# Optimization experiments

Measured on AMD Instinct MI355X. Metric: run time of the kernel, lower is better.

Reference implementation:

```python
import jax, jax.numpy as jnp
import numpy as np

K_NEIGH = 16  # ball-query neighborhood size


def pdist2(a, b):
    # (B,N,3),(B,M,3) -> (B,N,M) squared euclidean distances
    aa = jnp.sum(a * a, -1)[:, :, None]
    bb = jnp.sum(b * b, -1)[:, None, :]
    return jnp.maximum(aa + bb - 2.0 * jnp.einsum('bnd,bmd->bnm', a, b), 0.0)


def fps(xyz, npoint):
    # furthest point sampling, xyz (B,N,3) -> idx (B,npoint) int32
    B, N, _ = xyz.shape

    def body(carry, _):
        dist, far = carry
        centroid = xyz[jnp.arange(B), far]  # (B,3)
        d = jnp.sum((xyz - centroid[:, None, :]) ** 2, -1)
        dist = jnp.minimum(dist, d)
        nxt = jnp.argmax(dist, axis=1).astype(jnp.int32)
        return (dist, nxt), far

    init = (jnp.full((B, N), 1e10, xyz.dtype), jnp.zeros((B,), jnp.int32))
    _, idxs = jax.lax.scan(body, init, None, length=npoint)
    return idxs.T  # (B, npoint)


def gather(x, idx):
    # x (B,N,C), idx (B,S) -> (B,S,C)
    return jnp.take_along_axis(x, idx[:, :, None], axis=1)


def lae_conv(xyz, fea, W, b, A, radius):
    # LAE-Conv: ball-query (K nearest capped to radius, out-of-ball -> self),
    # pointwise feature transform, attention over neighbors from coord offsets.
    B, N, _ = xyz.shape
    d2 = pdist2(xyz, xyz)
    negd, idx = jax.lax.top_k(-d2, K_NEIGH)          # (B,N,K)
    in_ball = (-negd) <= radius * radius
    self_idx = jnp.broadcast_to(jnp.arange(N, dtype=idx.dtype)[None, :, None], idx.shape)
    idx = jnp.where(in_ball, idx, self_idx)
    g_xyz = jnp.take_along_axis(xyz[:, None], idx[..., None], axis=2) - xyz[:, :, None, :]  # (B,N,K,3)
    g_fea = jnp.take_along_axis(fea[:, None], idx[..., None], axis=2)                        # (B,N,K,Cin)
    h = jnp.einsum('bnkc,co->bnko', g_fea, W) + b    # (B,N,K,Cout)
    alpha = jax.nn.softmax(jnp.einsum('bnkd,d->bnk', g_xyz, A), axis=-1)
    return jax.nn.relu(jnp.einsum('bnk,bnko->bno', alpha, h))


def self_attn(fea, Wq, Wk, Wv):
    # non-local self-attention block with additive merge (PSAB)
    q, k, v = fea @ Wq, fea @ Wk, fea @ Wv
    a = jax.nn.softmax(jnp.einsum('bnc,bmc->bnm', q, k), axis=-1)
    return jnp.einsum('bnm,bmc->bnc', a, v) + fea


def fp_interp(xyz_d, xyz_s, fea_d, fea_s):
    # pointnet feature propagation: 3-NN inverse-distance interp + skip concat
    d2 = pdist2(xyz_d, xyz_s)
    negd, idx = jax.lax.top_k(-d2, 3)
    w = 1.0 / jnp.maximum(-negd, 1e-10)
    w = w / jnp.sum(w, -1, keepdims=True)
    g = jnp.take_along_axis(fea_s[:, None], idx[..., None], axis=2)  # (B,Nd,3,C)
    interp = jnp.einsum('bnk,bnkc->bnc', w, g)
    return jnp.concatenate([fea_d, interp], axis=-1)


def pan_forward(xyz, W0, b0, A0, W1, b1, A1, W2, b2, A2, W3, b3, A3, W4, b4, A4,
                W5, b5, A5, W6, b6, A6, Wq1, Wk1, Wv1, Wq2, Wk2, Wv2, Wq3, Wk3, Wv3, Wf, bf):
    fea0 = lae_conv(xyz, xyz, W0, b0, A0, 0.06)       # (B,N,64)
    idx1 = fps(xyz, 512)
    xyz1, fea1 = gather(xyz, idx1), gather(fea0, idx1)
    fea1 = lae_conv(xyz1, fea1, W1, b1, A1, 0.12)     # (B,512,128)
    idx2 = fps(xyz1, 128)
    xyz2, fea2 = gather(xyz1, idx2), gather(fea1, idx2)
    fea2 = lae_conv(xyz2, fea2, W2, b2, A2, 0.3)      # (B,128,256)
    fea2 = self_attn(fea2, Wq1, Wk1, Wv1)
    idx3 = fps(xyz2, 64)
    xyz3, fea3 = gather(xyz2, idx3), gather(fea2, idx3)
    fea3 = lae_conv(xyz3, fea3, W3, b3, A3, 0.5)      # (B,64,512)
    fea3 = self_attn(fea3, Wq2, Wk2, Wv2)
    fea2 = fp_interp(xyz2, xyz3, fea2, fea3)          # (B,128,768)
    fea2 = lae_conv(xyz2, fea2, W4, b4, A4, 0.3)      # (B,128,256)
    fea2 = self_attn(fea2, Wq3, Wk3, Wv3)
    fea1 = fp_interp(xyz1, xyz2, fea1, fea2)          # (B,512,384)
    fea1 = lae_conv(xyz1, fea1, W5, b5, A5, 0.12)     # (B,512,256)
    fea0 = fp_interp(xyz, xyz1, fea0, fea1)           # (B,N,320)
    fea0 = lae_conv(xyz, fea0, W6, b6, A6, 0.06)      # (B,N,128)
    out = fea0 @ Wf + bf                              # (B,N,num_class)
    return out.transpose(0, 2, 1)                     # (B,num_class,N)


def setup_inputs() -> dict:
    key = jax.random.key(0)
    B, N, NUM_CLASS = 4, 4096, 13
    ks = iter(jax.random.split(key, 64))

    def lin(cin, cout):
        return jax.random.normal(next(ks), (cin, cout), jnp.float32) / np.sqrt(cin).astype(np.float32)

    inp = {'xyz': jax.random.uniform(next(ks), (B, N, 3), jnp.float32)}
    lae_dims = [(3, 64), (64, 128), (128, 256), (256, 512), (768, 256), (384, 256), (320, 128)]
    for i, (ci, co) in enumerate(lae_dims):
        inp[f'W{i}'] = lin(ci, co)
        inp[f'b{i}'] = jnp.zeros((co,), jnp.float32)
        inp[f'A{i}'] = jax.random.normal(next(ks), (3,), jnp.float32)
    for j, c in zip((1, 2, 3), (256, 512, 256)):
        inp[f'Wq{j}'] = lin(c, c)
        inp[f'Wk{j}'] = lin(c, c)
        inp[f'Wv{j}'] = lin(c, c)
    inp['Wf'] = lin(128, NUM_CLASS)
    inp['bf'] = jnp.zeros((NUM_CLASS,), jnp.float32)
    return inp


def reference(xyz, W0, b0, A0, W1, b1, A1, W2, b2, A2, W3, b3, A3, W4, b4, A4,
              W5, b5, A5, W6, b6, A6, Wq1, Wk1, Wv1, Wq2, Wk2, Wv2, Wq3, Wk3, Wv3, Wf, bf):
    return pan_forward(xyz, W0, b0, A0, W1, b1, A1, W2, b2, A2, W3, b3, A3, W4, b4, A4,
                       W5, b5, A5, W6, b6, A6, Wq1, Wk1, Wv1, Wq2, Wk2, Wv2, Wq3, Wk3, Wv3, Wf, bf)
```

## Files before the change

### kernel.cpp

```cpp
#include <hip/hip_runtime.h>
#include <math.h>

#define NB 4

typedef unsigned long long u64;

#define CSWAP(a, b)                                          \
  {                                                          \
    u64 _mn = (b < a) ? b : a;                               \
    u64 _mx = (b < a) ? a : b;                               \
    a = _mn;                                                 \
    b = _mx;                                                 \
  }

__global__ __launch_bounds__(256) void norms_kernel(const float* __restrict__ xyz,
                                                    float4* __restrict__ xw, int total) {
#pragma clang fp contract(off)
  int i = blockIdx.x * 256 + threadIdx.x;
  if (i >= total) return;
  float x = xyz[3 * i + 0], y = xyz[3 * i + 1], z = xyz[3 * i + 2];
  xw[i] = make_float4(x, y, z, x * x + y * y + z * z);
}

__device__ __forceinline__ void knn16_search(const float4* __restrict__ xwb, int N, int n,
                                             int lane, u64* lists, u64* win) {
#pragma clang fp contract(off)
  float4 q = xwb[n];
  float qq = q.w;
  const u64 SENT = ((u64)0x7F800000u << 32) | (unsigned)lane;
  u64 k0 = SENT, k1 = SENT, k2 = SENT, k3 = SENT, k4 = SENT, k5 = SENT, k6 = SENT,
      k7 = SENT, k8 = SENT, k9 = SENT, k10 = SENT, k11 = SENT, k12 = SENT, k13 = SENT,
      k14 = SENT, k15 = SENT;
  int rounds = N >> 6;
  for (int j = 0; j < rounds; ++j) {
    int m = j * 64 + lane;
    float4 p = xwb[m];
    float ab = q.x * p.x + q.y * p.y + q.z * p.z;
    float d2 = fmaxf((qq + p.w) - 2.0f * ab, 0.0f);
    u64 key = ((u64)__float_as_uint(d2) << 32) | (unsigned)m;
    if (key < k15) {
      k15 = key;
      CSWAP(k14, k15); CSWAP(k13, k14); CSWAP(k12, k13); CSWAP(k11, k12);
      CSWAP(k10, k11); CSWAP(k9, k10);  CSWAP(k8, k9);   CSWAP(k7, k8);
      CSWAP(k6, k7);   CSWAP(k5, k6);   CSWAP(k4, k5);   CSWAP(k3, k4);
      CSWAP(k2, k3);   CSWAP(k1, k2);   CSWAP(k0, k1);
    }
  }
  lists[0 * 64 + lane] = k0;   lists[1 * 64 + lane] = k1;
  lists[2 * 64 + lane] = k2;   lists[3 * 64 + lane] = k3;
  lists[4 * 64 + lane] = k4;   lists[5 * 64 + lane] = k5;
  lists[6 * 64 + lane] = k6;   lists[7 * 64 + lane] = k7;
  lists[8 * 64 + lane] = k8;   lists[9 * 64 + lane] = k9;
  lists[10 * 64 + lane] = k10; lists[11 * 64 + lane] = k11;
  lists[12 * 64 + lane] = k12; lists[13 * 64 + lane] = k13;
  lists[14 * 64 + lane] = k14; lists[15 * 64 + lane] = k15;
  __syncthreads();
  int head = 0;
  u64 outk = 0;
  for (int r = 0; r < 16; ++r) {
    u64 h = lists[head * 64 + lane];
    u64 mn = h;
#pragma unroll
    for (int mask = 32; mask; mask >>= 1) {
      u64 o = __shfl_xor(mn, mask);
      if (o < mn) mn = o;
    }
    if (h == mn) head++;
    if (lane == r) outk = mn;
  }
  if (lane < 16) win[lane] = outk;
  __syncthreads();
}

__device__ __forceinline__ void lae_alphas(const float4* __restrict__ xwb, int n,
                                           const int* idv, const float* __restrict__ A,
                                           float* al) {
  float ax = A[0], ay = A[1], az = A[2];
  float4 q = xwb[n];
  float mx = -3.0e38f;
#pragma unroll
  for (int k = 0; k < 16; ++k) {
    float4 p = xwb[idv[k]];
    float gx = p.x - q.x, gy = p.y - q.y, gz = p.z - q.z;
    float s = gx * ax + gy * ay + gz * az;
    al[k] = s;
    mx = fmaxf(mx, s);
  }
  float sum = 0.0f;
#pragma unroll
  for (int k = 0; k < 16; ++k) { al[k] = expf(al[k] - mx); sum += al[k]; }
#pragma unroll
  for (int k = 0; k < 16; ++k) al[k] = al[k] / sum;
}

template <int NT, int PTS, int NPT>
__device__ __forceinline__ void fps_body(const float4* __restrict__ xw, int N, int npoint,
                                         int* __restrict__ idx_out,
                                         float4* __restrict__ xw_out, u64* smem, int b,
                                         int tid) {
#pragma clang fp contract(off)
  constexpr int NW = NT / 64;
  u64* rk = smem;
  int* hist = (int*)(smem + 2 * NW);
  float* sxyz = (float*)(hist + 512);
  const float4* xb = xw + (size_t)b * N;
  for (int i = tid; i < N; i += NT) {
    float4 p = xb[i];
    sxyz[3 * i + 0] = p.x;
    sxyz[3 * i + 1] = p.y;
    sxyz[3 * i + 2] = p.z;
  }
  float px[PTS], py[PTS], pz[PTS], dist[PTS];
#pragma unroll
  for (int p = 0; p < PTS; ++p) {
    float4 v = xb[tid + p * NT];
    px[p] = v.x;
    py[p] = v.y;
    pz[p] = v.z;
    dist[p] = 1e10f;
  }
  __syncthreads();
  int far = 0;
  float cx = sxyz[0], cy = sxyz[1], cz = sxyz[2];
  for (int t = 0; t < npoint; ++t) {
    if (tid == 0) hist[t] = far;
    u64 K[PTS];
#pragma unroll
    for (int p = 0; p < PTS; ++p) {
      float dx = px[p] - cx, dy = py[p] - cy, dz = pz[p] - cz;
      float d = dx * dx + dy * dy + dz * dz;
      float nd = fminf(dist[p], d);
      dist[p] = nd;
      K[p] = ((u64)__float_as_uint(nd) << 32) | (unsigned)(~(tid + p * NT));
    }
#pragma unroll
    for (int s = PTS / 2; s >= 1; s >>= 1) {
#pragma unroll
      for (int i = 0; i < s; ++i)
        if (K[i + s] > K[i]) K[i] = K[i + s];
    }
    u64 key = K[0];
#pragma unroll
    for (int m = 1; m <= 32; m <<= 1) {
      u64 o = __shfl_xor(key, m);
      if (o > key) key = o;
    }
    if constexpr (NW > 1) {
      int par = (t & 1) * NW;
      if ((tid & 63) == 0) rk[par + (tid >> 6)] = key;
      __syncthreads();
      key = rk[par + 0];
#pragma unroll
      for (int w = 1; w < NW; ++w)
        if (rk[par + w] > key) key = rk[par + w];
    }
    far = (int)(~(unsigned)key);
    cx = sxyz[3 * far + 0];
    cy = sxyz[3 * far + 1];
    cz = sxyz[3 * far + 2];
  }
  __syncthreads();
  for (int s = tid; s < npoint; s += NT) {
    int idp = hist[s];
    idx_out[(size_t)b * npoint + s] = idp;
    xw_out[(size_t)b * npoint + s] = xb[idp];
  }
}

__device__ __forceinline__ void knn_gw_body(const float4* __restrict__ xw_s, int N, float r2,
                                            int* __restrict__ idxK,
                                            const int* __restrict__ srcmap,
                                            const float* __restrict__ fea_src, int Nsrc,
                                            int Cin, const float* __restrict__ A,
                                            float* __restrict__ wf, int bn, int lane,
                                            u64* lists, u64* win) {
  int b = bn / N, n = bn - b * N;
  const float4* xb = xw_s + (size_t)b * N;
  knn16_search(xb, N, n, lane, lists, win);
  int idv[16];
#pragma unroll
  for (int k = 0; k < 16; ++k) {
    u64 kk = win[k];
    float d2 = __uint_as_float((unsigned)(kk >> 32));
    idv[k] = (d2 <= r2) ? (int)(kk & 0xFFFFFFFFu) : n;
  }
  if (lane < 16) idxK[(size_t)bn * 16 + lane] = idv[lane];
  float al[16];
  lae_alphas(xb, n, idv, A, al);
  int row[16];
  const int* sm = srcmap + (size_t)b * N;
#pragma unroll
  for (int k = 0; k < 16; ++k) row[k] = sm[idv[k]];
  const float* fb = fea_src + (size_t)b * Nsrc * Cin;
  float* wo = wf + (size_t)bn * Cin;
  for (int c = lane; c < Cin; c += 64) {
    float acc = 0.0f;
#pragma unroll
    for (int k = 0; k < 16; ++k) acc += al[k] * fb[(size_t)row[k] * Cin + c];
    wo[c] = acc;
  }
}

__device__ __forceinline__ void knn_gw0_body(const float4* __restrict__ xw, int N, float r2,
                                             int* __restrict__ idxK,
                                             const float* __restrict__ W0,
                                             const float* __restrict__ b0,
                                             const float* __restrict__ A0,
                                             float* __restrict__ fea0, int bn, int lane,
                                             u64* lists, u64* win) {
  int b = bn / N, n = bn - b * N;
  const float4* xb = xw + (size_t)b * N;
  knn16_search(xb, N, n, lane, lists, win);
  int idv[16];
#pragma unroll
  for (int k = 0; k < 16; ++k) {
    u64 kk = win[k];
    float d2 = __uint_as_float((unsigned)(kk >> 32));
    idv[k] = (d2 <= r2) ? (int)(kk & 0xFFFFFFFFu) : n;
  }
  if (lane < 16) idxK[(size_t)bn * 16 + lane] = idv[lane];
  float al[16];
  lae_alphas(xb, n, idv, A0, al);
  float w0 = 0.0f, w1 = 0.0f, w2 = 0.0f;
#pragma unroll
  for (int k = 0; k < 16; ++k) {
    float4 p = xb[idv[k]];
    w0 += al[k] * p.x;
    w1 += al[k] * p.y;
    w2 += al[k] * p.z;
  }
  float v = w0 * W0[0 * 64 + lane] + w1 * W0[1 * 64 + lane] + w2 * W0[2 * 64 + lane] +
            b0[lane];
  fea0[(size_t)bn * 64 + lane] = fmaxf(v, 0.0f);
}

__device__ __forceinline__ void interp3_body(const float4* __restrict__ xd,
                                             const float4* __restrict__ xs, int Nd, int Ns,
                                             int* __restrict__ idx3, float* __restrict__ w3,
                                             int gid) {
#pragma clang fp contract(off)
  int b = gid / Nd;
  const float4* xb = xs + (size_t)b * Ns;
  float4 q = xd[gid];
  float qq = q.w;
  float v0 = 3.0e38f, v1 = 3.0e38f, v2 = 3.0e38f;
  int i0 = 0, i1 = 0, i2 = 0;
  for (int m = 0; m < Ns; ++m) {
    float4 p = xb[m];
    float ab = q.x * p.x + q.y * p.y + q.z * p.z;
    float d2 = fmaxf((qq + p.w) - 2.0f * ab, 0.0f);
    if (d2 < v2) {
      if (d2 < v0) { v2 = v1; i2 = i1; v1 = v0; i1 = i0; v0 = d2; i0 = m; }
      else if (d2 < v1) { v2 = v1; i2 = i1; v1 = d2; i1 = m; }
      else { v2 = d2; i2 = m; }
    }
  }
  float w0 = 1.0f / fmaxf(v0, 1e-10f);
  float w1 = 1.0f / fmaxf(v1, 1e-10f);
  float w2 = 1.0f / fmaxf(v2, 1e-10f);
  float s = w0 + w1 + w2;
  idx3[gid * 3 + 0] = i0; idx3[gid * 3 + 1] = i1; idx3[gid * 3 + 2] = i2;
  w3[gid * 3 + 0] = w0 / s; w3[gid * 3 + 1] = w1 / s; w3[gid * 3 + 2] = w2 / s;
}

__global__ __launch_bounds__(256) void combo_A_kernel(
    const float4* __restrict__ xw0, float r2, int* __restrict__ idxK0,
    const float* __restrict__ W0, const float* __restrict__ b0,
    const float* __restrict__ A0, float* __restrict__ fea0, int* __restrict__ idx1,
    float4* __restrict__ xw1) {
  __shared__ u64 smem[6432];
  if (blockIdx.x < NB) {
    fps_body<256, 16, 4096>(xw0, 4096, 512, idx1, xw1, smem, blockIdx.x, threadIdx.x);
  } else {
    int wave = threadIdx.x >> 6, lane = threadIdx.x & 63;
    int bn = (blockIdx.x - NB) * 4 + wave;
    knn_gw0_body(xw0, 4096, r2, idxK0, W0, b0, A0, fea0, bn, lane, smem + (size_t)wave * 1024,
                 smem + 4096 + wave * 16);
  }
}

__global__ __launch_bounds__(64) void combo_B_kernel(
    const float4* __restrict__ xw0, const float4* __restrict__ xw1, float r2,
    int* __restrict__ idxK1, const int* __restrict__ idx1, const float* __restrict__ fea0,
    const float* __restrict__ A1, float* __restrict__ wf, int* __restrict__ idx2,
    float4* __restrict__ xw2, int* __restrict__ idxI0, float* __restrict__ wI0) {
  __shared__ u64 smem[1056];
  int bid = blockIdx.x;
  if (bid < NB) {
    fps_body<64, 8, 512>(xw1, 512, 128, idx2, xw2, smem, bid, threadIdx.x);
  } else if (bid < NB + NB * 512) {
    knn_gw_body(xw1, 512, r2, idxK1, idx1, fea0, 4096, 64, A1, wf, bid - NB, threadIdx.x,
                smem, smem + 1024);
  } else {
    int gid = (bid - NB - NB * 512) * 64 + threadIdx.x;
    interp3_body(xw0, xw1, 4096, 512, idxI0, wI0, gid);
  }
}

__global__ __launch_bounds__(64) void combo_D_kernel(
    const float4* __restrict__ xw1, const float4* __restrict__ xw2, float r2,
    int* __restrict__ idxK2, const int* __restrict__ idx2, const float* __restrict__ fea1,
    const float* __restrict__ A2, float* __restrict__ wf, int* __restrict__ idx3,
    float4* __restrict__ xw3, int* __restrict__ idxI1, float* __restrict__ wI1) {
  __shared__ u64 smem[1056];
  int bid = blockIdx.x;
  if (bid < NB) {
    fps_body<64, 2, 128>(xw2, 128, 64, idx3, xw3, smem, bid, threadIdx.x);
  } else if (bid < NB + NB * 128) {
    knn_gw_body(xw2, 128, r2, idxK2, idx2, fea1, 512, 128, A2, wf, bid - NB, threadIdx.x,
                smem, smem + 1024);
  } else {
    int gid = (bid - NB - NB * 128) * 64 + threadIdx.x;
    interp3_body(xw1, xw2, 512, 128, idxI1, wI1, gid);
  }
}

__global__ __launch_bounds__(64) void combo_H_kernel(
    const float4* __restrict__ xw2, const float4* __restrict__ xw3, float r2,
    int* __restrict__ idxK3, const int* __restrict__ idx3, const float* __restrict__ fea2b,
    const float* __restrict__ A3, float* __restrict__ wf, int* __restrict__ idxI2,
    float* __restrict__ wI2) {
  __shared__ u64 smem[1056];
  int bid = blockIdx.x;
  if (bid < NB * 64) {
    knn_gw_body(xw3, 64, r2, idxK3, idx3, fea2b, 128, 256, A3, wf, bid, threadIdx.x, smem,
                smem + 1024);
  } else {
    int gid = (bid - NB * 64) * 64 + threadIdx.x;
    interp3_body(xw2, xw3, 128, 64, idxI2, wI2, gid);
  }
}

__global__ __launch_bounds__(64) void gwpost_kernel(const float4* __restrict__ xw,
                                                    const float* __restrict__ Y,
                                                    const int* __restrict__ knn,
                                                    const float* __restrict__ A,
                                                    const float* __restrict__ bias,
                                                    float* __restrict__ out, int N, int C) {
  int bn = blockIdx.x;
  int b = bn / N, n = bn - b * N;
  int lane = threadIdx.x;
  const float4* xb = xw + (size_t)b * N;
  const int* kn = knn + (size_t)bn * 16;
  int idv[16];
#pragma unroll
  for (int k = 0; k < 16; ++k) idv[k] = kn[k];
  float al[16];
  lae_alphas(xb, n, idv, A, al);
  const float* Yb = Y + (size_t)b * N * C;
  float* wo = out + (size_t)bn * C;
  for (int c = lane; c < C; c += 64) {
    float acc = 0.0f;
#pragma unroll
    for (int k = 0; k < 16; ++k) acc += al[k] * Yb[(size_t)idv[k] * C + c];
    wo[c] = fmaxf(acc + bias[c], 0.0f);
  }
}

__global__ __launch_bounds__(64) void gwpost_final_kernel(
    const float4* __restrict__ xw, const float* __restrict__ Y, const int* __restrict__ knn,
    const float* __restrict__ A, const float* __restrict__ bias,
    const float* __restrict__ Wf, const float* __restrict__ bfv, float* __restrict__ out,
    int N) {
  int bn = blockIdx.x;
  int b = bn / N, n = bn - b * N;
  int lane = threadIdx.x;
  const float4* xb = xw + (size_t)b * N;
  const int* kn = knn + (size_t)bn * 16;
  int idv[16];
#pragma unroll
  for (int k = 0; k < 16; ++k) idv[k] = kn[k];
  float al[16];
  lae_alphas(xb, n, idv, A, al);
  const float* Yb = Y + (size_t)b * N * 128;
  float a0 = 0.0f, a1 = 0.0f;
#pragma unroll
  for (int k = 0; k < 16; ++k) {
    const float* yr = Yb + (size_t)idv[k] * 128;
    a0 += al[k] * yr[lane];
    a1 += al[k] * yr[lane + 64];
  }
  float v0 = fmaxf(a0 + bias[lane], 0.0f);
  float v1 = fmaxf(a1 + bias[lane + 64], 0.0f);
  float* ob = out + ((size_t)b * 13) * N + n;
#pragma unroll
  for (int cls = 0; cls < 13; ++cls) {
    float p = v0 * Wf[lane * 13 + cls] + v1 * Wf[(lane + 64) * 13 + cls];
#pragma unroll
    for (int m = 32; m; m >>= 1) p += __shfl_xor(p, m);
    if (lane == 0) ob[(size_t)cls * N] = p + bfv[cls];
  }
}

__device__ __forceinline__ void gemm_body(const float* __restrict__ Amat,
                                          const float* __restrict__ W,
                                          const float* __restrict__ bias,
                                          float* __restrict__ out, int K, int Cout, int relu,
                                          const int* __restrict__ i3,
                                          const float* __restrict__ w3,
                                          const float* __restrict__ Zb, int Nd, int Ns,
                                          float* lds_a) {
  int co = blockIdx.x * 64 + (threadIdx.x & 63);
  int rg = threadIdx.x >> 6;
  int r0 = blockIdx.y * 32;
  float acc[8];
#pragma unroll
  for (int j = 0; j < 8; ++j) acc[j] = 0.0f;
  for (int k0 = 0; k0 < K; k0 += 32) {
    int row = threadIdx.x >> 3;
    int kq = (threadIdx.x & 7) * 4;
    int gk = k0 + kq;
    const float* ap = Amat + (size_t)(r0 + row) * K + gk;
    float a0 = 0.0f, a1 = 0.0f, a2 = 0.0f, a3 = 0.0f;
    if (gk + 3 < K) {
      float4 tv = *(const float4*)ap;
      a0 = tv.x; a1 = tv.y; a2 = tv.z; a3 = tv.w;
    } else {
      if (gk + 0 < K) a0 = ap[0];
      if (gk + 1 < K) a1 = ap[1];
      if (gk + 2 < K) a2 = ap[2];
    }
    __syncthreads();
    lds_a[(kq + 0) * 36 + row] = a0;
    lds_a[(kq + 1) * 36 + row] = a1;
    lds_a[(kq + 2) * 36 + row] = a2;
    lds_a[(kq + 3) * 36 + row] = a3;
    __syncthreads();
    int kmax = K - k0;
    if (kmax > 32) kmax = 32;
    if (kmax == 32) {
#pragma unroll
      for (int kk = 0; kk < 32; ++kk) {
        float w = W[(size_t)(k0 + kk) * Cout + co];
        const float* ar = &lds_a[kk * 36 + rg * 8];
        float4 x0 = *(const float4*)ar;
        float4 x1 = *(const float4*)(ar + 4);
        acc[0] += x0.x * w; acc[1] += x0.y * w; acc[2] += x0.z * w; acc[3] += x0.w * w;
        acc[4] += x1.x * w; acc[5] += x1.y * w; acc[6] += x1.z * w; acc[7] += x1.w * w;
      }
    } else {
      for (int kk = 0; kk < kmax; ++kk) {
        float w = W[(size_t)(k0 + kk) * Cout + co];
        const float* ar = &lds_a[kk * 36 + rg * 8];
        float4 x0 = *(const float4*)ar;
        float4 x1 = *(const float4*)(ar + 4);
        acc[0] += x0.x * w; acc[1] += x0.y * w; acc[2] += x0.z * w; acc[3] += x0.w * w;
        acc[4] += x1.x * w; acc[5] += x1.y * w; acc[6] += x1.z * w; acc[7] += x1.w * w;
      }
    }
  }
  float bb = bias ? bias[co] : 0.0f;
#pragma unroll
  for (int j = 0; j < 8; ++j) {
    int r = r0 + rg * 8 + j;
    float vv = acc[j] + bb;
    if (i3) {
      int bidx = r / Nd;
      const int* ii = i3 + (size_t)r * 3;
      const float* ww = w3 + (size_t)r * 3;
      const float* zb = Zb + (size_t)bidx * Ns * Cout;
      vv += ww[0] * zb[(size_t)ii[0] * Cout + co] + ww[1] * zb[(size_t)ii[1] * Cout + co] +
            ww[2] * zb[(size_t)ii[2] * Cout + co];
    }
    if (relu) vv = fmaxf(vv, 0.0f);
    out[(size_t)r * Cout + co] = vv;
  }
}

__global__ __launch_bounds__(256) void gemm_kernel(const float* __restrict__ Amat,
                                                   const float* __restrict__ W,
                                                   const float* __restrict__ bias,
                                                   float* __restrict__ out, int K, int Cout,
                                                   int relu, const int* __restrict__ i3,
                                                   const float* __restrict__ w3,
                                                   const float* __restrict__ Zb, int Nd,
                                                   int Ns) {
  __shared__ float lds_a[32 * 36];
  gemm_body(Amat, W, bias, out, K, Cout, relu, i3, w3, Zb, Nd, Ns, lds_a);
}

__global__ __launch_bounds__(256) void gemm_qkv_kernel(
    const float* __restrict__ Amat, const float* __restrict__ Wq,
    const float* __restrict__ Wk, const float* __restrict__ Wv, float* __restrict__ oq,
    float* __restrict__ ok, float* __restrict__ ov, int K, int Cout) {
  __shared__ float lds_a[32 * 36];
  const float* W = blockIdx.z == 0 ? Wq : (blockIdx.z == 1 ? Wk : Wv);
  float* o = blockIdx.z == 0 ? oq : (blockIdx.z == 1 ? ok : ov);
  gemm_body(Amat, W, nullptr, o, K, Cout, 0, nullptr, nullptr, nullptr, 0, 0, lds_a);
}

__global__ __launch_bounds__(128) void attn_kernel(const float* __restrict__ q,
                                                   const float* __restrict__ k,
                                                   const float* __restrict__ v,
                                                   const float* __restrict__ fea,
                                                   float* __restrict__ out, int N, int C) {
  __shared__ float sa[128];
  __shared__ float sb[128];
  int b = blockIdx.y, n = blockIdx.x, t = threadIdx.x;
  const float* qn = q + ((size_t)b * N + n) * C;
  if (t < N) {
    const float4* km = (const float4*)(k + ((size_t)b * N + t) * C);
    const float4* q4 = (const float4*)qn;
    float acc = 0.0f;
    int C4 = C >> 2;
    for (int c = 0; c < C4; ++c) {
      float4 kv = km[c];
      float4 qv = q4[c];
      acc += qv.x * kv.x + qv.y * kv.y + qv.z * kv.z + qv.w * kv.w;
    }
    sa[t] = acc;
  }
  __syncthreads();
  float mx = -3.0e38f;
  for (int i = 0; i < N; ++i) mx = fmaxf(mx, sa[i]);
  if (t < N) sb[t] = expf(sa[t] - mx);
  __syncthreads();
  float sum = 0.0f;
  for (int i = 0; i < N; ++i) sum += sb[i];
  size_t rowo = ((size_t)b * N + n) * C;
  for (int c = t; c < C; c += 128) {
    float acc = 0.0f;
    for (int m = 0; m < N; ++m) acc += sb[m] * v[((size_t)b * N + m) * C + c];
    out[rowo + c] = acc / sum + fea[rowo + c];
  }
}

extern "C" void kernel_launch(void* const* d_in, const int* in_sizes, int n_in,
                              void* d_out, int out_size, void* d_ws, size_t ws_size,
                              hipStream_t stream) {
  (void)in_sizes; (void)n_in; (void)out_size; (void)ws_size;
  const float* xyz = (const float*)d_in[0];
  const float* W[7]; const float* bi[7]; const float* A[7];
  for (int i = 0; i < 7; ++i) {
    W[i] = (const float*)d_in[1 + 3 * i];
    bi[i] = (const float*)d_in[2 + 3 * i];
    A[i] = (const float*)d_in[3 + 3 * i];
  }
  const float* Wq1 = (const float*)d_in[22];
  const float* Wk1 = (const float*)d_in[23];
  const float* Wv1 = (const float*)d_in[24];
  const float* Wq2 = (const float*)d_in[25];
  const float* Wk2 = (const float*)d_in[26];
  const float* Wv2 = (const float*)d_in[27];
  const float* Wq3 = (const float*)d_in[28];
  const float* Wk3 = (const float*)d_in[29];
  const float* Wv3 = (const float*)d_in[30];
  const float* Wf = (const float*)d_in[31];
  const float* bf = (const float*)d_in[32];
  float* out = (float*)d_out;

  const int B = NB, N0 = 4096, N1 = 512, N2 = 128, N3 = 64;
  char* base = (char*)d_ws;
  size_t off = 0;
  auto alloc = [&](size_t bytes) -> void* {
    void* p = base + off;
    off += (bytes + 255) & ~(size_t)255;
    return p;
  };
  float4* xw0 = (float4*)alloc((size_t)B * N0 * 16);
  float4* xw1 = (float4*)alloc((size_t)B * N1 * 16);
  float4* xw2 = (float4*)alloc((size_t)B * N2 * 16);
  float4* xw3 = (float4*)alloc((size_t)B * N3 * 16);
  int* idxK0 = (int*)alloc((size_t)B * N0 * 16 * 4);
  int* idxK1 = (int*)alloc((size_t)B * N1 * 16 * 4);
  int* idxK2 = (int*)alloc((size_t)B * N2 * 16 * 4);
  int* idxK3 = (int*)alloc((size_t)B * N3 * 16 * 4);
  int* idx1 = (int*)alloc((size_t)B * N1 * 4);
  int* idx2 = (int*)alloc((size_t)B * N2 * 4);
  int* idx3 = (int*)alloc((size_t)B * N3 * 4);
  float* fea0 = (float*)alloc((size_t)B * N0 * 64 * 4);
  float* fea1 = (float*)alloc((size_t)B * N1 * 128 * 4);
  float* fea1b = (float*)alloc((size_t)B * N1 * 256 * 4);
  float* fea2a = (float*)alloc((size_t)B * N2 * 256 * 4);
  float* fea2b = (float*)alloc((size_t)B * N2 * 256 * 4);
  float* fea2c = (float*)alloc((size_t)B * N2 * 256 * 4);
  float* fea2d = (float*)alloc((size_t)B * N2 * 256 * 4);
  float* fea3a = (float*)alloc((size_t)B * N3 * 512 * 4);
  float* fea3b = (float*)alloc((size_t)B * N3 * 512 * 4);
  float* qb = (float*)alloc((size_t)B * 32768 * 4);
  float* kb = (float*)alloc((size_t)B * 32768 * 4);
  float* vb = (float*)alloc((size_t)B * 32768 * 4);
  int* idxI2 = (int*)alloc((size_t)B * N2 * 3 * 4);
  float* wI2 = (float*)alloc((size_t)B * N2 * 3 * 4);
  int* idxI1 = (int*)alloc((size_t)B * N1 * 3 * 4);
  float* wI1 = (float*)alloc((size_t)B * N1 * 3 * 4);
  int* idxI0 = (int*)alloc((size_t)B * N0 * 3 * 4);
  float* wI0 = (float*)alloc((size_t)B * N0 * 3 * 4);
  float* Zb4 = (float*)alloc((size_t)B * N3 * 256 * 4);
  float* Zb5 = (float*)alloc((size_t)B * N2 * 256 * 4);
  float* Zb6 = (float*)alloc((size_t)B * N1 * 128 * 4);
  float* Y4 = (float*)alloc((size_t)B * N2 * 256 * 4);
  float* Y5 = (float*)alloc((size_t)B * N1 * 256 * 4);
  float* Y6 = (float*)alloc((size_t)B * N0 * 128 * 4);
  float* wfb = (float*)alloc((size_t)B * N0 * 320 * 4);

  float r2_0 = (float)(0.06 * 0.06);
  float r2_1 = (float)(0.12 * 0.12);
  float r2_2 = (float)(0.3 * 0.3);
  float r2_3 = (float)(0.5 * 0.5);

  norms_kernel<<<B * N0 / 256, 256, 0, stream>>>(xyz, xw0, B * N0);

  combo_A_kernel<<<B + B * N0 / 4, 256, 0, stream>>>(xw0, r2_0, idxK0, W[0], bi[0], A[0],
                                                     fea0, idx1, xw1);
  combo_B_kernel<<<B + B * N1 + B * N0 / 64, 64, 0, stream>>>(
      xw0, xw1, r2_1, idxK1, idx1, fea0, A[1], wfb, idx2, xw2, idxI0, wI0);
  gemm_kernel<<<dim3(2, B * N1 / 32), 256, 0, stream>>>(wfb, W[1], bi[1], fea1, 64, 128, 1,
                                                        nullptr, nullptr, nullptr, 0, 0);
  combo_D_kernel<<<B + B * N2 + B * N1 / 64, 64, 0, stream>>>(
      xw1, xw2, r2_2, idxK2, idx2, fea1, A[2], wfb, idx3, xw3, idxI1, wI1);
  gemm_kernel<<<dim3(4, B * N2 / 32), 256, 0, stream>>>(wfb, W[2], bi[2], fea2a, 128, 256, 1,
                                                        nullptr, nullptr, nullptr, 0, 0);
  gemm_qkv_kernel<<<dim3(4, B * N2 / 32, 3), 256, 0, stream>>>(fea2a, Wq1, Wk1, Wv1, qb, kb,
                                                               vb, 256, 256);
  attn_kernel<<<dim3(N2, B), 128, 0, stream>>>(qb, kb, vb, fea2a, fea2b, N2, 256);

  combo_H_kernel<<<B * N3 + B * N2 / 64, 64, 0, stream>>>(xw2, xw3, r2_3, idxK3, idx3, fea2b,
                                                          A[3], wfb, idxI2, wI2);
  gemm_kernel<<<dim3(8, B * N3 / 32), 256, 0, stream>>>(wfb, W[3], bi[3], fea3a, 256, 512, 1,
                                                        nullptr, nullptr, nullptr, 0, 0);
  gemm_qkv_kernel<<<dim3(8, B * N3 / 32, 3), 256, 0, stream>>>(fea3a, Wq2, Wk2, Wv2, qb, kb,
                                                               vb, 512, 512);
  attn_kernel<<<dim3(N3, B), 128, 0, stream>>>(qb, kb, vb, fea3a, fea3b, N3, 512);

  gemm_kernel<<<dim3(4, B * N3 / 32), 256, 0, stream>>>(fea3b, W[4] + 256 * 256, nullptr, Zb4,
                                                        512, 256, 0, nullptr, nullptr,
                                                        nullptr, 0, 0);
  gemm_kernel<<<dim3(4, B * N2 / 32), 256, 0, stream>>>(fea2b, W[4], nullptr, Y4, 256, 256, 0,
                                                        idxI2, wI2, Zb4, N2, N3);
  gwpost_kernel<<<B * N2, 64, 0, stream>>>(xw2, Y4, idxK2, A[4], bi[4], fea2c, N2, 256);
  gemm_qkv_kernel<<<dim3(4, B * N2 / 32, 3), 256, 0, stream>>>(fea2c, Wq3, Wk3, Wv3, qb, kb,
                                                               vb, 256, 256);
  attn_kernel<<<dim3(N2, B), 128, 0, stream>>>(qb, kb, vb, fea2c, fea2d, N2, 256);

  gemm_kernel<<<dim3(4, B * N2 / 32), 256, 0, stream>>>(fea2d, W[5] + 128 * 256, nullptr, Zb5,
                                                        256, 256, 0, nullptr, nullptr,
                                                        nullptr, 0, 0);
  gemm_kernel<<<dim3(4, B * N1 / 32), 256, 0, stream>>>(fea1, W[5], nullptr, Y5, 128, 256, 0,
                                                        idxI1, wI1, Zb5, N1, N2);
  gwpost_kernel<<<B * N1, 64, 0, stream>>>(xw1, Y5, idxK1, A[5], bi[5], fea1b, N1, 256);

  gemm_kernel<<<dim3(2, B * N1 / 32), 256, 0, stream>>>(fea1b, W[6] + 64 * 128, nullptr, Zb6,
                                                        256, 128, 0, nullptr, nullptr,
                                                        nullptr, 0, 0);
  gemm_kernel<<<dim3(2, B * N0 / 32), 256, 0, stream>>>(fea0, W[6], nullptr, Y6, 64, 128, 0,
                                                        idxI0, wI0, Zb6, N0, N1);
  gwpost_final_kernel<<<B * N0, 64, 0, stream>>>(xw0, Y6, idxK0, A[6], bi[6], Wf, bf, out,
                                                 N0);
}
```

Baseline: 916.2 us.

## Hoist skip-branch GEMMs into earlier combo kernels and rework FPS argmax

The skip-connection GEMMs (fea0·W6a, fea1·W5a, fea2b·W4a) move out of the decoder and run as extra blocks inside the earlier combo kernels, where they overlap with FPS and kNN work. The interpolation add becomes a separate elementwise kernel applied after the coarse GEMM. Combo B, D and H switch to 256-thread blocks with four waves each. FPS now gives each thread a contiguous run of points and finds the argmax with a float max-shuffle plus a ballot, instead of reducing packed 64-bit keys. The cost is three extra launches and an extra read-modify-write pass over Y.

Result: faster. 861.1 us, median of 2 (-6.0%).

```diff
diff --git a/kernel.cpp b/kernel.cpp
--- a/kernel.cpp
+++ b/kernel.cpp
@@ -100,6 +100,7 @@
                                          int tid) {
 #pragma clang fp contract(off)
   constexpr int NW = NT / 64;
+  constexpr bool FULL = (NT * PTS == NPT);
   u64* rk = smem;
   int* hist = (int*)(smem + 2 * NW);
   float* sxyz = (float*)(hist + 512);
@@ -113,10 +114,13 @@
   float px[PTS], py[PTS], pz[PTS], dist[PTS];
 #pragma unroll
   for (int p = 0; p < PTS; ++p) {
-    float4 v = xb[tid + p * NT];
-    px[p] = v.x;
-    py[p] = v.y;
-    pz[p] = v.z;
+    int pt = tid * PTS + p;
+    if (FULL || pt < N) {
+      float4 v = xb[pt];
+      px[p] = v.x;
+      py[p] = v.y;
+      pz[p] = v.z;
+    }
     dist[p] = 1e10f;
   }
   __syncthreads();
@@ -124,35 +128,38 @@
   float cx = sxyz[0], cy = sxyz[1], cz = sxyz[2];
   for (int t = 0; t < npoint; ++t) {
     if (tid == 0) hist[t] = far;
-    u64 K[PTS];
+    float bestd = -1.0f;
+    int bestp = 0;
 #pragma unroll
     for (int p = 0; p < PTS; ++p) {
-      float dx = px[p] - cx, dy = py[p] - cy, dz = pz[p] - cz;
-      float d = dx * dx + dy * dy + dz * dz;
-      float nd = fminf(dist[p], d);
-      dist[p] = nd;
-      K[p] = ((u64)__float_as_uint(nd) << 32) | (unsigned)(~(tid + p * NT));
-    }
-#pragma unroll
-    for (int s = PTS / 2; s >= 1; s >>= 1) {
-#pragma unroll
-      for (int i = 0; i < s; ++i)
-        if (K[i + s] > K[i]) K[i] = K[i + s];
-    }
-    u64 key = K[0];
-#pragma unroll
-    for (int m = 1; m <= 32; m <<= 1) {
-      u64 o = __shfl_xor(key, m);
-      if (o > key) key = o;
-    }
+      int pt = tid * PTS + p;
+      if (FULL || pt < N) {
+        float dx = px[p] - cx, dy = py[p] - cy, dz = pz[p] - cz;
+        float d = dx * dx + dy * dy + dz * dz;
+        float nd = fminf(dist[p], d);
+        dist[p] = nd;
+        if (nd > bestd) { bestd = nd; bestp = pt; }
+      }
+    }
+    float wmax = bestd;
+#pragma unroll
+    for (int m = 1; m <= 32; m <<= 1) wmax = fmaxf(wmax, __shfl_xor(wmax, m));
+    u64 mask = __ballot(bestd == wmax);
+    int wl = __ffsll(mask) - 1;
+    int widx = __shfl(bestp, wl);
+    u64 key = (wmax < 0.0f)
+                  ? 0ull
+                  : (((u64)__float_as_uint(wmax) << 32) | (unsigned)(~widx));
     if constexpr (NW > 1) {
       int par = (t & 1) * NW;
       if ((tid & 63) == 0) rk[par + (tid >> 6)] = key;
       __syncthreads();
       key = rk[par + 0];
 #pragma unroll
-      for (int w = 1; w < NW; ++w)
-        if (rk[par + w] > key) key = rk[par + w];
+      for (int w = 1; w < NW; ++w) {
+        u64 o = rk[par + w];
+        if (o > key) key = o;
+      }
     }
     far = (int)(~(unsigned)key);
     cx = sxyz[3 * far + 0];
@@ -263,146 +270,14 @@
   w3[gid * 3 + 0] = w0 / s; w3[gid * 3 + 1] = w1 / s; w3[gid * 3 + 2] = w2 / s;
 }
 
-__global__ __launch_bounds__(256) void combo_A_kernel(
-    const float4* __restrict__ xw0, float r2, int* __restrict__ idxK0,
-    const float* __restrict__ W0, const float* __restrict__ b0,
-    const float* __restrict__ A0, float* __restrict__ fea0, int* __restrict__ idx1,
-    float4* __restrict__ xw1) {
-  __shared__ u64 smem[6432];
-  if (blockIdx.x < NB) {
-    fps_body<256, 16, 4096>(xw0, 4096, 512, idx1, xw1, smem, blockIdx.x, threadIdx.x);
-  } else {
-    int wave = threadIdx.x >> 6, lane = threadIdx.x & 63;
-    int bn = (blockIdx.x - NB) * 4 + wave;
-    knn_gw0_body(xw0, 4096, r2, idxK0, W0, b0, A0, fea0, bn, lane, smem + (size_t)wave * 1024,
-                 smem + 4096 + wave * 16);
-  }
-}
-
-__global__ __launch_bounds__(64) void combo_B_kernel(
-    const float4* __restrict__ xw0, const float4* __restrict__ xw1, float r2,
-    int* __restrict__ idxK1, const int* __restrict__ idx1, const float* __restrict__ fea0,
-    const float* __restrict__ A1, float* __restrict__ wf, int* __restrict__ idx2,
-    float4* __restrict__ xw2, int* __restrict__ idxI0, float* __restrict__ wI0) {
-  __shared__ u64 smem[1056];
-  int bid = blockIdx.x;
-  if (bid < NB) {
-    fps_body<64, 8, 512>(xw1, 512, 128, idx2, xw2, smem, bid, threadIdx.x);
-  } else if (bid < NB + NB * 512) {
-    knn_gw_body(xw1, 512, r2, idxK1, idx1, fea0, 4096, 64, A1, wf, bid - NB, threadIdx.x,
-                smem, smem + 1024);
-  } else {
-    int gid = (bid - NB - NB * 512) * 64 + threadIdx.x;
-    interp3_body(xw0, xw1, 4096, 512, idxI0, wI0, gid);
-  }
-}
-
-__global__ __launch_bounds__(64) void combo_D_kernel(
-    const float4* __restrict__ xw1, const float4* __restrict__ xw2, float r2,
-    int* __restrict__ idxK2, const int* __restrict__ idx2, const float* __restrict__ fea1,
-    const float* __restrict__ A2, float* __restrict__ wf, int* __restrict__ idx3,
-    float4* __restrict__ xw3, int* __restrict__ idxI1, float* __restrict__ wI1) {
-  __shared__ u64 smem[1056];
-  int bid = blockIdx.x;
-  if (bid < NB) {
-    fps_body<64, 2, 128>(xw2, 128, 64, idx3, xw3, smem, bid, threadIdx.x);
-  } else if (bid < NB + NB * 128) {
-    knn_gw_body(xw2, 128, r2, idxK2, idx2, fea1, 512, 128, A2, wf, bid - NB, threadIdx.x,
-                smem, smem + 1024);
-  } else {
-    int gid = (bid - NB - NB * 128) * 64 + threadIdx.x;
-    interp3_body(xw1, xw2, 512, 128, idxI1, wI1, gid);
-  }
-}
-
-__global__ __launch_bounds__(64) void combo_H_kernel(
-    const float4* __restrict__ xw2, const float4* __restrict__ xw3, float r2,
-    int* __restrict__ idxK3, const int* __restrict__ idx3, const float* __restrict__ fea2b,
-    const float* __restrict__ A3, float* __restrict__ wf, int* __restrict__ idxI2,
-    float* __restrict__ wI2) {
-  __shared__ u64 smem[1056];
-  int bid = blockIdx.x;
-  if (bid < NB * 64) {
-    knn_gw_body(xw3, 64, r2, idxK3, idx3, fea2b, 128, 256, A3, wf, bid, threadIdx.x, smem,
-                smem + 1024);
-  } else {
-    int gid = (bid - NB * 64) * 64 + threadIdx.x;
-    interp3_body(xw2, xw3, 128, 64, idxI2, wI2, gid);
-  }
-}
-
-__global__ __launch_bounds__(64) void gwpost_kernel(const float4* __restrict__ xw,
-                                                    const float* __restrict__ Y,
-                                                    const int* __restrict__ knn,
-                                                    const float* __restrict__ A,
-                                                    const float* __restrict__ bias,
-                                                    float* __restrict__ out, int N, int C) {
-  int bn = blockIdx.x;
-  int b = bn / N, n = bn - b * N;
-  int lane = threadIdx.x;
-  const float4* xb = xw + (size_t)b * N;
-  const int* kn = knn + (size_t)bn * 16;
-  int idv[16];
-#pragma unroll
-  for (int k = 0; k < 16; ++k) idv[k] = kn[k];
-  float al[16];
-  lae_alphas(xb, n, idv, A, al);
-  const float* Yb = Y + (size_t)b * N * C;
-  float* wo = out + (size_t)bn * C;
-  for (int c = lane; c < C; c += 64) {
-    float acc = 0.0f;
-#pragma unroll
-    for (int k = 0; k < 16; ++k) acc += al[k] * Yb[(size_t)idv[k] * C + c];
-    wo[c] = fmaxf(acc + bias[c], 0.0f);
-  }
-}
-
-__global__ __launch_bounds__(64) void gwpost_final_kernel(
-    const float4* __restrict__ xw, const float* __restrict__ Y, const int* __restrict__ knn,
-    const float* __restrict__ A, const float* __restrict__ bias,
-    const float* __restrict__ Wf, const float* __restrict__ bfv, float* __restrict__ out,
-    int N) {
-  int bn = blockIdx.x;
-  int b = bn / N, n = bn - b * N;
-  int lane = threadIdx.x;
-  const float4* xb = xw + (size_t)b * N;
-  const int* kn = knn + (size_t)bn * 16;
-  int idv[16];
-#pragma unroll
-  for (int k = 0; k < 16; ++k) idv[k] = kn[k];
-  float al[16];
-  lae_alphas(xb, n, idv, A, al);
-  const float* Yb = Y + (size_t)b * N * 128;
-  float a0 = 0.0f, a1 = 0.0f;
-#pragma unroll
-  for (int k = 0; k < 16; ++k) {
-    const float* yr = Yb + (size_t)idv[k] * 128;
-    a0 += al[k] * yr[lane];
-    a1 += al[k] * yr[lane + 64];
-  }
-  float v0 = fmaxf(a0 + bias[lane], 0.0f);
-  float v1 = fmaxf(a1 + bias[lane + 64], 0.0f);
-  float* ob = out + ((size_t)b * 13) * N + n;
-#pragma unroll
-  for (int cls = 0; cls < 13; ++cls) {
-    float p = v0 * Wf[lane * 13 + cls] + v1 * Wf[(lane + 64) * 13 + cls];
-#pragma unroll
-    for (int m = 32; m; m >>= 1) p += __shfl_xor(p, m);
-    if (lane == 0) ob[(size_t)cls * N] = p + bfv[cls];
-  }
-}
-
-__device__ __forceinline__ void gemm_body(const float* __restrict__ Amat,
+__device__ __forceinline__ void gemm_body(int bx, int by, const float* __restrict__ Amat,
                                           const float* __restrict__ W,
                                           const float* __restrict__ bias,
                                           float* __restrict__ out, int K, int Cout, int relu,
-                                          const int* __restrict__ i3,
-                                          const float* __restrict__ w3,
-                                          const float* __restrict__ Zb, int Nd, int Ns,
                                           float* lds_a) {
-  int co = blockIdx.x * 64 + (threadIdx.x & 63);
+  int co = bx * 64 + (threadIdx.x & 63);
   int rg = threadIdx.x >> 6;
-  int r0 = blockIdx.y * 32;
+  int r0 = by * 32;
   float acc[8];
 #pragma unroll
   for (int j = 0; j < 8; ++j) acc[j] = 0.0f;
@@ -454,14 +329,6 @@
   for (int j = 0; j < 8; ++j) {
     int r = r0 + rg * 8 + j;
     float vv = acc[j] + bb;
-    if (i3) {
-      int bidx = r / Nd;
-      const int* ii = i3 + (size_t)r * 3;
-      const float* ww = w3 + (size_t)r * 3;
-      const float* zb = Zb + (size_t)bidx * Ns * Cout;
-      vv += ww[0] * zb[(size_t)ii[0] * Cout + co] + ww[1] * zb[(size_t)ii[1] * Cout + co] +
-            ww[2] * zb[(size_t)ii[2] * Cout + co];
-    }
     if (relu) vv = fmaxf(vv, 0.0f);
     out[(size_t)r * Cout + co] = vv;
   }
@@ -471,12 +338,9 @@
                                                    const float* __restrict__ W,
                                                    const float* __restrict__ bias,
                                                    float* __restrict__ out, int K, int Cout,
-                                                   int relu, const int* __restrict__ i3,
-                                                   const float* __restrict__ w3,
-                                                   const float* __restrict__ Zb, int Nd,
-                                                   int Ns) {
+                                                   int relu) {
   __shared__ float lds_a[32 * 36];
-  gemm_body(Amat, W, bias, out, K, Cout, relu, i3, w3, Zb, Nd, Ns, lds_a);
+  gemm_body(blockIdx.x, blockIdx.y, Amat, W, bias, out, K, Cout, relu, lds_a);
 }
 
 __global__ __launch_bounds__(256) void gemm_qkv_kernel(
@@ -486,7 +350,170 @@
   __shared__ float lds_a[32 * 36];
   const float* W = blockIdx.z == 0 ? Wq : (blockIdx.z == 1 ? Wk : Wv);
   float* o = blockIdx.z == 0 ? oq : (blockIdx.z == 1 ? ok : ov);
-  gemm_body(Amat, W, nullptr, o, K, Cout, 0, nullptr, nullptr, nullptr, 0, 0, lds_a);
+  gemm_body(blockIdx.x, blockIdx.y, Amat, W, nullptr, o, K, Cout, 0, lds_a);
+}
+
+__global__ __launch_bounds__(256) void interp_add_kernel(float* __restrict__ Y,
+                                                         const int* __restrict__ i3,
+                                                         const float* __restrict__ w3,
+                                                         const float* __restrict__ Zb,
+                                                         int Nd, int Ns, int C, int total) {
+  int gid = blockIdx.x * 256 + threadIdx.x;
+  if (gid >= total) return;
+  int c = gid % C;
+  int r = gid / C;
+  int b = r / Nd;
+  const int* ii = i3 + (size_t)r * 3;
+  const float* ww = w3 + (size_t)r * 3;
+  const float* zb = Zb + (size_t)b * Ns * C;
+  Y[gid] += ww[0] * zb[(size_t)ii[0] * C + c] + ww[1] * zb[(size_t)ii[1] * C + c] +
+            ww[2] * zb[(size_t)ii[2] * C + c];
+}
+
+__global__ __launch_bounds__(256) void combo_A_kernel(
+    const float4* __restrict__ xw0, float r2, int* __restrict__ idxK0,
+    const float* __restrict__ W0, const float* __restrict__ b0,
+    const float* __restrict__ A0, float* __restrict__ fea0, int* __restrict__ idx1,
+    float4* __restrict__ xw1) {
+  __shared__ u64 smem[6432];
+  if (blockIdx.x < NB) {
+    fps_body<256, 16, 4096>(xw0, 4096, 512, idx1, xw1, smem, blockIdx.x, threadIdx.x);
+  } else {
+    int wave = threadIdx.x >> 6, lane = threadIdx.x & 63;
+    int bn = (blockIdx.x - NB) * 4 + wave;
+    knn_gw0_body(xw0, 4096, r2, idxK0, W0, b0, A0, fea0, bn, lane, smem + (size_t)wave * 1024,
+                 smem + 4096 + wave * 16);
+  }
+}
+
+__global__ __launch_bounds__(256) void combo_B_kernel(
+    const float4* __restrict__ xw0, const float4* __restrict__ xw1, float r2,
+    int* __restrict__ idxK1, const int* __restrict__ idx1, const float* __restrict__ fea0,
+    const float* __restrict__ A1, float* __restrict__ wf, int* __restrict__ idx2,
+    float4* __restrict__ xw2, int* __restrict__ idxI0, float* __restrict__ wI0,
+    const float* __restrict__ W6a, float* __restrict__ Y6) {
+  __shared__ u64 smem[4160];
+  int bid = blockIdx.x;
+  if (bid < NB) {
+    fps_body<256, 2, 512>(xw1, 512, 128, idx2, xw2, smem, bid, threadIdx.x);
+  } else if (bid < NB + 512) {
+    int wave = threadIdx.x >> 6, lane = threadIdx.x & 63;
+    int bn = (bid - NB) * 4 + wave;
+    knn_gw_body(xw1, 512, r2, idxK1, idx1, fea0, 4096, 64, A1, wf, bn, lane,
+                smem + (size_t)wave * 1024, smem + 4096 + wave * 16);
+  } else if (bid < NB + 512 + 64) {
+    int gid = (bid - NB - 512) * 256 + threadIdx.x;
+    interp3_body(xw0, xw1, 4096, 512, idxI0, wI0, gid);
+  } else {
+    int gb = bid - (NB + 512 + 64);
+    gemm_body(gb & 1, gb >> 1, fea0, W6a, nullptr, Y6, 64, 128, 0, (float*)smem);
+  }
+}
+
+__global__ __launch_bounds__(256) void combo_D_kernel(
+    const float4* __restrict__ xw1, const float4* __restrict__ xw2, float r2,
+    int* __restrict__ idxK2, const int* __restrict__ idx2, const float* __restrict__ fea1,
+    const float* __restrict__ A2, float* __restrict__ wf, int* __restrict__ idx3,
+    float4* __restrict__ xw3, int* __restrict__ idxI1, float* __restrict__ wI1,
+    const float* __restrict__ W5a, float* __restrict__ Y5) {
+  __shared__ u64 smem[4160];
+  int bid = blockIdx.x;
+  if (bid < NB) {
+    fps_body<256, 1, 128>(xw2, 128, 64, idx3, xw3, smem, bid, threadIdx.x);
+  } else if (bid < NB + 128) {
+    int wave = threadIdx.x >> 6, lane = threadIdx.x & 63;
+    int bn = (bid - NB) * 4 + wave;
+    knn_gw_body(xw2, 128, r2, idxK2, idx2, fea1, 512, 128, A2, wf, bn, lane,
+                smem + (size_t)wave * 1024, smem + 4096 + wave * 16);
+  } else if (bid < NB + 128 + 8) {
+    int gid = (bid - NB - 128) * 256 + threadIdx.x;
+    interp3_body(xw1, xw2, 512, 128, idxI1, wI1, gid);
+  } else {
+    int gb = bid - (NB + 128 + 8);
+    gemm_body(gb & 3, gb >> 2, fea1, W5a, nullptr, Y5, 128, 256, 0, (float*)smem);
+  }
+}
+
+__global__ __launch_bounds__(256) void combo_H_kernel(
+    const float4* __restrict__ xw2, const float4* __restrict__ xw3, float r2,
+    int* __restrict__ idxK3, const int* __restrict__ idx3, const float* __restrict__ fea2b,
+    const float* __restrict__ A3, float* __restrict__ wf, int* __restrict__ idxI2,
+    float* __restrict__ wI2, const float* __restrict__ W4a, float* __restrict__ Y4) {
+  __shared__ u64 smem[4160];
+  int bid = blockIdx.x;
+  if (bid < 64) {
+    int wave = threadIdx.x >> 6, lane = threadIdx.x & 63;
+    int bn = bid * 4 + wave;
+    knn_gw_body(xw3, 64, r2, idxK3, idx3, fea2b, 128, 256, A3, wf, bn, lane,
+                smem + (size_t)wave * 1024, smem + 4096 + wave * 16);
+  } else if (bid < 64 + 2) {
+    int gid = (bid - 64) * 256 + threadIdx.x;
+    interp3_body(xw2, xw3, 128, 64, idxI2, wI2, gid);
+  } else {
+    int gb = bid - 66;
+    gemm_body(gb & 3, gb >> 2, fea2b, W4a, nullptr, Y4, 256, 256, 0, (float*)smem);
+  }
+}
+
+__global__ __launch_bounds__(64) void gwpost_kernel(const float4* __restrict__ xw,
+                                                    const float* __restrict__ Y,
+                                                    const int* __restrict__ knn,
+                                                    const float* __restrict__ A,
+                                                    const float* __restrict__ bias,
+                                                    float* __restrict__ out, int N, int C) {
+  int bn = blockIdx.x;
+  int b = bn / N, n = bn - b * N;
+  int lane = threadIdx.x;
+  const float4* xb = xw + (size_t)b * N;
+  const int* kn = knn + (size_t)bn * 16;
+  int idv[16];
+#pragma unroll
+  for (int k = 0; k < 16; ++k) idv[k] = kn[k];
+  float al[16];
+  lae_alphas(xb, n, idv, A, al);
+  const float* Yb = Y + (size_t)b * N * C;
+  float* wo = out + (size_t)bn * C;
+  for (int c = lane; c < C; c += 64) {
+    float acc = 0.0f;
+#pragma unroll
+    for (int k = 0; k < 16; ++k) acc += al[k] * Yb[(size_t)idv[k] * C + c];
+    wo[c] = fmaxf(acc + bias[c], 0.0f);
+  }
+}
+
+__global__ __launch_bounds__(64) void gwpost_final_kernel(
+    const float4* __restrict__ xw, const float* __restrict__ Y, const int* __restrict__ knn,
+    const float* __restrict__ A, const float* __restrict__ bias,
+    const float* __restrict__ Wf, const float* __restrict__ bfv, float* __restrict__ out,
+    int N) {
+  int bn = blockIdx.x;
+  int b = bn / N, n = bn - b * N;
+  int lane = threadIdx.x;
+  const float4* xb = xw + (size_t)b * N;
+  const int* kn = knn + (size_t)bn * 16;
+  int idv[16];
+#pragma unroll
+  for (int k = 0; k < 16; ++k) idv[k] = kn[k];
+  float al[16];
+  lae_alphas(xb, n, idv, A, al);
+  const float* Yb = Y + (size_t)b * N * 128;
+  float a0 = 0.0f, a1 = 0.0f;
+#pragma unroll
+  for (int k = 0; k < 16; ++k) {
+    const float* yr = Yb + (size_t)idv[k] * 128;
+    a0 += al[k] * yr[lane];
+    a1 += al[k] * yr[lane + 64];
+  }
+  float v0 = fmaxf(a0 + bias[lane], 0.0f);
+  float v1 = fmaxf(a1 + bias[lane + 64], 0.0f);
+  float* ob = out + ((size_t)b * 13) * N + n;
+#pragma unroll
+  for (int cls = 0; cls < 13; ++cls) {
+    float p = v0 * Wf[lane * 13 + cls] + v1 * Wf[(lane + 64) * 13 + cls];
+#pragma unroll
+    for (int m = 32; m; m >>= 1) p += __shfl_xor(p, m);
+    if (lane == 0) ob[(size_t)cls * N] = p + bfv[cls];
+  }
 }
 
 __global__ __launch_bounds__(128) void attn_kernel(const float* __restrict__ q,
@@ -603,48 +630,42 @@
 
   combo_A_kernel<<<B + B * N0 / 4, 256, 0, stream>>>(xw0, r2_0, idxK0, W[0], bi[0], A[0],
                                                      fea0, idx1, xw1);
-  combo_B_kernel<<<B + B * N1 + B * N0 / 64, 64, 0, stream>>>(
-      xw0, xw1, r2_1, idxK1, idx1, fea0, A[1], wfb, idx2, xw2, idxI0, wI0);
-  gemm_kernel<<<dim3(2, B * N1 / 32), 256, 0, stream>>>(wfb, W[1], bi[1], fea1, 64, 128, 1,
-                                                        nullptr, nullptr, nullptr, 0, 0);
-  combo_D_kernel<<<B + B * N2 + B * N1 / 64, 64, 0, stream>>>(
-      xw1, xw2, r2_2, idxK2, idx2, fea1, A[2], wfb, idx3, xw3, idxI1, wI1);
-  gemm_kernel<<<dim3(4, B * N2 / 32), 256, 0, stream>>>(wfb, W[2], bi[2], fea2a, 128, 256, 1,
-                                                        nullptr, nullptr, nullptr, 0, 0);
+  combo_B_kernel<<<NB + 512 + 64 + 1024, 256, 0, stream>>>(
+      xw0, xw1, r2_1, idxK1, idx1, fea0, A[1], wfb, idx2, xw2, idxI0, wI0, W[6], Y6);
+  gemm_kernel<<<dim3(2, B * N1 / 32), 256, 0, stream>>>(wfb, W[1], bi[1], fea1, 64, 128, 1);
+  combo_D_kernel<<<NB + 128 + 8 + 256, 256, 0, stream>>>(
+      xw1, xw2, r2_2, idxK2, idx2, fea1, A[2], wfb, idx3, xw3, idxI1, wI1, W[5], Y5);
+  gemm_kernel<<<dim3(4, B * N2 / 32), 256, 0, stream>>>(wfb, W[2], bi[2], fea2a, 128, 256, 1);
   gemm_qkv_kernel<<<dim3(4, B * N2 / 32, 3), 256, 0, stream>>>(fea2a, Wq1, Wk1, Wv1, qb, kb,
                                                                vb, 256, 256);
   attn_kernel<<<dim3(N2, B), 128, 0, stream>>>(qb, kb, vb, fea2a, fea2b, N2, 256);
 
-  combo_H_kernel<<<B * N3 + B * N2 / 64, 64, 0, stream>>>(xw2, xw3, r2_3, idxK3, idx3, fea2b,
-                                                          A[3], wfb, idxI2, wI2);
-  gemm_kernel<<<dim3(8, B * N3 / 32), 256, 0, stream>>>(wfb, W[3], bi[3], fea3a, 256, 512, 1,
-                                                        nullptr, nullptr, nullptr, 0, 0);
+  combo_H_kernel<<<64 + 2 + 64, 256, 0, stream>>>(xw2, xw3, r2_3, idxK3, idx3, fea2b, A[3],
+                                                  wfb, idxI2, wI2, W[4], Y4);
+  gemm_kernel<<<dim3(8, B * N3 / 32), 256, 0, stream>>>(wfb, W[3], bi[3], fea3a, 256, 512, 1);
   gemm_qkv_kernel<<<dim3(8, B * N3 / 32, 3), 256, 0, stream>>>(fea3a, Wq2, Wk2, Wv2, qb, kb,
                                                                vb, 512, 512);
   attn_kernel<<<dim3(N3, B), 128, 0, stream>>>(qb, kb, vb, fea3a, fea3b, N3, 512);
 
   gemm_kernel<<<dim3(4, B * N3 / 32), 256, 0, stream>>>(fea3b, W[4] + 256 * 256, nullptr, Zb4,
-                                                        512, 256, 0, nullptr, nullptr,
-                                                        nullptr, 0, 0);
-  gemm_kernel<<<dim3(4, B * N2 / 32), 256, 0, stream>>>(fea2b, W[4], nullptr, Y4, 256, 256, 0,
-                                                        idxI2, wI2, Zb4, N2, N3);
+                                                        512, 256, 0);
+  interp_add_kernel<<<B * N2 * 256 / 256, 256, 0, stream>>>(Y4, idxI2, wI2, Zb4, N2, N3, 256,
+                                                            B * N2 * 256);
   gwpost_kernel<<<B * N2, 64, 0, stream>>>(xw2, Y4, idxK2, A[4], bi[4], fea2c, N2, 256);
   gemm_qkv_kernel<<<dim3(4, B * N2 / 32, 3), 256, 0, stream>>>(fea2c, Wq3, Wk3, Wv3, qb, kb,
                                                                vb, 256, 256);
   attn_kernel<<<dim3(N2, B), 128, 0, stream>>>(qb, kb, vb, fea2c, fea2d, N2, 256);
 
   gemm_kernel<<<dim3(4, B * N2 / 32), 256, 0, stream>>>(fea2d, W[5] + 128 * 256, nullptr, Zb5,
-                                                        256, 256, 0, nullptr, nullptr,
-                                                        nullptr, 0, 0);
-  gemm_kernel<<<dim3(4, B * N1 / 32), 256, 0, stream>>>(fea1, W[5], nullptr, Y5, 128, 256, 0,
-                                                        idxI1, wI1, Zb5, N1, N2);
+                                                        256, 256, 0);
+  interp_add_kernel<<<B * N1 * 256 / 256, 256, 0, stream>>>(Y5, idxI1, wI1, Zb5, N1, N2, 256,
+                                                            B * N1 * 256);
   gwpost_kernel<<<B * N1, 64, 0, stream>>>(xw1, Y5, idxK1, A[5], bi[5], fea1b, N1, 256);
 
   gemm_kernel<<<dim3(2, B * N1 / 32), 256, 0, stream>>>(fea1b, W[6] + 64 * 128, nullptr, Zb6,
-                                                        256, 128, 0, nullptr, nullptr,
-                                                        nullptr, 0, 0);
-  gemm_kernel<<<dim3(2, B * N0 / 32), 256, 0, stream>>>(fea0, W[6], nullptr, Y6, 64, 128, 0,
-                                                        idxI0, wI0, Zb6, N0, N1);
+                                                        256, 128, 0);
+  interp_add_kernel<<<B * N0 * 128 / 256, 256, 0, stream>>>(Y6, idxI0, wI0, Zb6, N0, N1, 128,
+                                                            B * N0 * 128);
   gwpost_final_kernel<<<B * N0, 64, 0, stream>>>(xw0, Y6, idxK0, A[6], bi[6], Wf, bf, out,
                                                  N0);
 }
```
